# Kernel tuning notes

Hardware: AMD Instinct MI355X
Metric: run time of the kernel (lower is better)

Reference implementation:

```python
import jax, jax.numpy as jnp
import numpy as np

B, T, C, V = 4, 2048, 512, 32000


def setup_inputs() -> dict:
    key = jax.random.key(0)
    ks = jax.random.split(key, 8)
    return {
        "idx": jax.random.randint(ks[0], (B, T), 0, V, dtype=jnp.int64 if jax.config.jax_enable_x64 else jnp.int32),
        "targets": jax.random.randint(ks[1], (B, T), 0, V, dtype=jnp.int64 if jax.config.jax_enable_x64 else jnp.int32),
        "token_emb": jax.random.normal(ks[2], (V, C), jnp.float32) * 0.02,
        "pos_emb": jax.random.normal(ks[3], (T, C), jnp.float32) * 0.02,
        "Wk": jax.random.normal(ks[4], (C, C), jnp.float32) / np.sqrt(C),
        "Wq": jax.random.normal(ks[5], (C, C), jnp.float32) / np.sqrt(C),
        "Wv": jax.random.normal(ks[6], (C, C), jnp.float32) / np.sqrt(C),
        "Wo": jax.random.normal(ks[7], (C, V), jnp.float32) / np.sqrt(C),
        "bo": jnp.zeros((V,), jnp.float32),
    }


def reference(idx, targets, token_emb, pos_emb, Wk, Wq, Wv, Wo, bo):
    # embeddings: token lookup + positional add  -> [B, T, C]
    x = token_emb[idx] + pos_emb[None, :idx.shape[1]]
    # single self-attention head (scale uses input dim C, per source)
    q = x @ Wq  # [B, T, C]
    k = x @ Wk
    v = x @ Wv
    wei = jnp.einsum("btc,bsc->bts", q, k) * (C ** -0.5)  # [B, T, T]
    mask = jnp.tril(jnp.ones((idx.shape[1], idx.shape[1]), bool))
    wei = jnp.where(mask[None], wei, -jnp.inf)
    wei = jax.nn.softmax(wei, axis=-1)
    attn = jnp.einsum("bts,bsc->btc", wei, v)  # [B, T, C]
    logits = attn @ Wo + bo  # [B, T, V]
    # cross-entropy (mean over B*T), matching F.cross_entropy
    logp = jax.nn.log_softmax(logits, axis=-1)
    nll = -jnp.take_along_axis(logp, targets[..., None], axis=-1)[..., 0]
    loss = nll.mean()
    return logits, loss
```

## Files before the change

kernel.cpp:

```cpp
#include <hip/hip_runtime.h>
#include <cstdint>

typedef unsigned short u16;
typedef __attribute__((ext_vector_type(8))) short short8;
typedef __attribute__((ext_vector_type(4))) float f32x4;

constexpr int kB = 4, kT = 2048, kC = 512, kV = 32000;
constexpr int kBT = kB * kT;
constexpr float kScale = 0.044194173824159216f;

__device__ __forceinline__ u16 f2b(float f) {
  union { float f; unsigned u; } v; v.f = f;
  unsigned r = v.u + 0x7fffu + ((v.u >> 16) & 1u);
  return (u16)(r >> 16);
}

__device__ __forceinline__ void g2lds16(const u16* g, u16* l) {
  __builtin_amdgcn_global_load_lds(
      (const __attribute__((address_space(1))) void*)g,
      (__attribute__((address_space(3))) void*)l, 16, 0, 0);
}

__global__ __launch_bounds__(256) void transpose_cast(const float* __restrict__ in,
                                                      u16* __restrict__ out,
                                                      int R, int Ncol) {
  __shared__ u16 tile[32][33];
  int c0 = blockIdx.x * 32, r0 = blockIdx.y * 32;
  int tx = threadIdx.x, ty = threadIdx.y;
#pragma unroll
  for (int j = 0; j < 32; j += 8)
    tile[ty + j][tx] = f2b(in[(long)(r0 + ty + j) * Ncol + (c0 + tx)]);
  __syncthreads();
#pragma unroll
  for (int j = 0; j < 32; j += 8)
    out[(long)(c0 + ty + j) * R + (r0 + tx)] = tile[tx][ty + j];
}

__global__ __launch_bounds__(128) void embed_kernel(const int* __restrict__ idx,
                                                    const float* __restrict__ te,
                                                    const float* __restrict__ pe,
                                                    u16* __restrict__ xb) {
  int row = blockIdx.x;
  int t = row & (kT - 1);
  int tok = idx[row];
  int c = threadIdx.x * 4;
  float4 a = *(const float4*)(te + (long)tok * kC + c);
  float4 p = *(const float4*)(pe + (long)t * kC + c);
  ushort4 o;
  o.x = f2b(a.x + p.x); o.y = f2b(a.y + p.y);
  o.z = f2b(a.z + p.z); o.w = f2b(a.w + p.w);
  *(ushort4*)(xb + (long)row * kC + c) = o;
}

template <int OUT_MODE, bool CAUSAL>
__global__ __launch_bounds__(256) void gemm_bt(
    const u16* __restrict__ A, const u16* __restrict__ Bt, void* __restrict__ OutP,
    const float* __restrict__ bias,
    int M, int N, int K, int lda, int ldb, int ldo,
    long batchA, long batchB, long batchO, float alpha) {
  int bz = blockIdx.z;
  A += bz * batchA;
  Bt += bz * batchB;
  int m0 = blockIdx.y * 128, n0 = blockIdx.x * 128;
  if (CAUSAL && n0 > m0 + 127) return;

  __shared__ u16 As[2][128 * 32];
  __shared__ u16 Bs[2][128 * 32];
  int tid = threadIdx.x;
  int lane = tid & 63, w = tid >> 6;
  int wr = w >> 1, wc = w & 1;
  int lm = lane & 15, lk = lane >> 4;

  f32x4 acc[4][4] = {};

  const u16* aptr = A + (long)(m0 + (w << 4) + (lane >> 2)) * lda + ((lane & 3) << 3);
  const u16* bptr = Bt + (long)(n0 + (w << 4) + (lane >> 2)) * ldb + ((lane & 3) << 3);

#define STAGE(buf)                                                   \
  {                                                                  \
    g2lds16(aptr,                  &As[buf][(w << 4) * 32]);         \
    g2lds16(aptr + (long)64 * lda, &As[buf][(64 + (w << 4)) * 32]);  \
    g2lds16(bptr,                  &Bs[buf][(w << 4) * 32]);         \
    g2lds16(bptr + (long)64 * ldb, &Bs[buf][(64 + (w << 4)) * 32]);  \
  }

  int nk = K >> 5;
  STAGE(0);
  __syncthreads();

  for (int kt = 0; kt < nk; ++kt) {
    int cur = kt & 1;
    aptr += 32; bptr += 32;
    if (kt + 1 < nk) STAGE(cur ^ 1);
    short8 af[4], bf[4];
#pragma unroll
    for (int i = 0; i < 4; ++i) {
      af[i] = *(const short8*)&As[cur][(wr * 64 + i * 16 + lm) * 32 + lk * 8];
      bf[i] = *(const short8*)&Bs[cur][(wc * 64 + i * 16 + lm) * 32 + lk * 8];
    }
#pragma unroll
    for (int mi = 0; mi < 4; ++mi)
#pragma unroll
      for (int ni = 0; ni < 4; ++ni)
        acc[mi][ni] = __builtin_amdgcn_mfma_f32_16x16x32_bf16(af[mi], bf[ni], acc[mi][ni], 0, 0, 0);
    __syncthreads();
  }
#undef STAGE

#pragma unroll
  for (int mi = 0; mi < 4; ++mi) {
#pragma unroll
    for (int ni = 0; ni < 4; ++ni) {
      int row = m0 + wr * 64 + mi * 16 + lk * 4;
      int col = n0 + wc * 64 + ni * 16 + lm;
      if (OUT_MODE == 0) {
        float* Out = (float*)OutP + bz * batchO;
        float bv = bias ? bias[col] : 0.0f;
#pragma unroll
        for (int r = 0; r < 4; ++r)
          Out[(long)(row + r) * ldo + col] = acc[mi][ni][r] * alpha + bv;
      } else if (OUT_MODE == 1) {
        u16* Out = (u16*)OutP + bz * batchO;
#pragma unroll
        for (int r = 0; r < 4; ++r)
          Out[(long)(row + r) * ldo + col] = f2b(acc[mi][ni][r] * alpha);
      } else {
        u16* Out = (u16*)OutP + bz * batchO;
        ushort4 pk;
        pk.x = f2b(acc[mi][ni][0] * alpha);
        pk.y = f2b(acc[mi][ni][1] * alpha);
        pk.z = f2b(acc[mi][ni][2] * alpha);
        pk.w = f2b(acc[mi][ni][3] * alpha);
        *(ushort4*)&Out[(long)col * ldo + row] = pk;
      }
    }
  }
}

__global__ __launch_bounds__(512, 2) void gemm256_logits_ce(
    const u16* __restrict__ A, const u16* __restrict__ Bt,
    float* __restrict__ Out, const float* __restrict__ bias,
    float2* __restrict__ cepart) {
  constexpr int lda = kC, ldb = kC, ldo = kV;
  constexpr int nk = kC / 64;
  constexpr int NB = kV / 256;

  __shared__ u16 lds[65536];

  int wg = blockIdx.x;
  int swzb = (wg & 7) * (gridDim.x >> 3) + (wg >> 3);
  int bx = swzb % NB, by = swzb / NB;
  int m0 = by * 256, n0 = bx * 256;

  int tid = threadIdx.x;
  int lane = tid & 63, w = tid >> 6;
  int wm = w >> 2, wn = w & 3;
  int lm = lane & 15, lk = lane >> 4;
  int lk16 = lk * 16, sw = (lm & 7) << 4;
  int brow0 = (wn & 1) * 64;

  int srow = tid >> 3;
  int scol = ((tid & 7) ^ ((tid >> 3) & 7)) * 8;
  const u16* Arow = A + (long)(m0 + srow) * lda + scol;
  const u16* Brow = Bt + (long)(n0 + srow) * ldb + scol;

  f32x4 acc[8][4] = {};
  short8 aF[4][2], bF[4][2];

  auto stage = [&](int s) {
    if (s >= 4 * nk) return;
    int tile = s >> 2, hf = s & 3, buf = tile & 1;
    int kofs = tile * 64;
    if (hf >= 2) {
      u16* base = &lds[(buf * 2 + (hf - 2)) * 8192 + w * 512];
      const u16* g = Arow + (long)((hf - 2) * 128) * lda + kofs;
      g2lds16(g, base);
      g2lds16(g + (long)64 * lda, base + 4096);
    } else {
      u16* base = &lds[32768 + (buf * 2 + hf) * 8192 + w * 512];
      const u16* g = Brow + (long)(hf * 128) * ldb + kofs;
      g2lds16(g, base);
      g2lds16(g + (long)64 * ldb, base + 4096);
    }
  };

#pragma unroll
  for (int s = 0; s < 6; ++s) stage(s);
  asm volatile("s_waitcnt vmcnt(4)" ::: "memory");
  __builtin_amdgcn_sched_barrier(0);
  __builtin_amdgcn_s_barrier();

#pragma unroll 2
  for (int t = 0; t < nk; ++t) {
    int cur = t & 1;
    const char* Ab = (const char*)&lds[(cur * 2 + wm) * 8192];
    const char* Bb = (const char*)&lds[32768 + (cur * 2 + (wn >> 1)) * 8192];

#define RDA(i, ks) (*(const short8*)(Ab + (((qr)*4 + (i)) * 16 + lm) * 128 + (((ks)*64 + lk16) ^ sw)))
#define RDB(j, ks) (*(const short8*)(Bb + (brow0 + ((qc)*2 + (j)) * 16 + lm) * 128 + (((ks)*64 + lk16) ^ sw)))
#define MFMA_QUAD                                                              \
  _Pragma("unroll") for (int i = 0; i < 4; ++i)                                \
  _Pragma("unroll") for (int j = 0; j < 2; ++j)                                \
  _Pragma("unroll") for (int ks = 0; ks < 2; ++ks)                             \
      acc[qr * 4 + i][qc * 2 + j] = __builtin_amdgcn_mfma_f32_16x16x32_bf16(   \
          aF[i][ks], bF[qc * 2 + j][ks], acc[qr * 4 + i][qc * 2 + j], 0, 0, 0);

    {
      constexpr int qr = 0, qc = 0;
#pragma unroll
      for (int i = 0; i < 4; ++i) { aF[i][0] = RDA(i, 0); aF[i][1] = RDA(i, 1); }
#pragma unroll
      for (int j = 0; j < 2; ++j) { bF[j][0] = RDB(j, 0); bF[j][1] = RDB(j, 1); }
      stage(4 * (t + 1) + 2);
      stage(4 * (t + 1) + 3);
      __builtin_amdgcn_s_barrier();
      asm volatile("s_waitcnt lgkmcnt(0)" ::: "memory");
      __builtin_amdgcn_s_setprio(1);
      MFMA_QUAD
      __builtin_amdgcn_s_setprio(0);
      __builtin_amdgcn_s_barrier();
    }
    {
      constexpr int qr = 0, qc = 1;
#pragma unroll
      for (int j = 0; j < 2; ++j) { bF[2 + j][0] = RDB(j, 0); bF[2 + j][1] = RDB(j, 1); }
      __builtin_amdgcn_s_barrier();
      asm volatile("s_waitcnt lgkmcnt(0)" ::: "memory");
      __builtin_amdgcn_s_setprio(1);
      MFMA_QUAD
      __builtin_amdgcn_s_setprio(0);
      __builtin_amdgcn_s_barrier();
    }
    {
      constexpr int qr = 1, qc = 0;
#pragma unroll
      for (int i = 0; i < 4; ++i) { aF[i][0] = RDA(i, 0); aF[i][1] = RDA(i, 1); }
      __builtin_amdgcn_s_barrier();
      asm volatile("s_waitcnt lgkmcnt(0)" ::: "memory");
      __builtin_amdgcn_s_setprio(1);
      MFMA_QUAD
      __builtin_amdgcn_s_setprio(0);
      __builtin_amdgcn_s_barrier();
    }
    {
      constexpr int qr = 1, qc = 1;
      stage(4 * (t + 2) + 0);
      stage(4 * (t + 2) + 1);
      __builtin_amdgcn_s_barrier();
      asm volatile("s_waitcnt lgkmcnt(0)" ::: "memory");
      __builtin_amdgcn_s_setprio(1);
      MFMA_QUAD
      __builtin_amdgcn_s_setprio(0);
      if (t < nk - 2) {
        asm volatile("s_waitcnt vmcnt(4)" ::: "memory");
        __builtin_amdgcn_sched_barrier(0);
      } else if (t == nk - 2) {
        asm volatile("s_waitcnt vmcnt(0)" ::: "memory");
        __builtin_amdgcn_sched_barrier(0);
      }
      __builtin_amdgcn_s_barrier();
    }
#undef RDA
#undef RDB
#undef MFMA_QUAD
  }

  float2* lds_ce = (float2*)lds;
#pragma unroll
  for (int rf = 0; rf < 8; ++rf) {
    int grow = m0 + wm * 128 + rf * 16 + lk * 4;
    float rm[4], rs[4];
#pragma unroll
    for (int r = 0; r < 4; ++r) { rm[r] = -1e30f; rs[r] = 0.0f; }
#pragma unroll
    for (int cf = 0; cf < 4; ++cf) {
      int col = n0 + wn * 64 + cf * 16 + lm;
      float bv = bias[col];
#pragma unroll
      for (int r = 0; r < 4; ++r) {
        float v = acc[rf][cf][r] + bv;
        Out[(long)(grow + r) * ldo + col] = v;
        float M = fmaxf(rm[r], v);
        rs[r] = rs[r] * __expf(rm[r] - M) + __expf(v - M);
        rm[r] = M;
      }
    }
#pragma unroll
    for (int off = 1; off < 16; off <<= 1) {
#pragma unroll
      for (int r = 0; r < 4; ++r) {
        float om = __shfl_xor(rm[r], off, 64);
        float os = __shfl_xor(rs[r], off, 64);
        float M = fmaxf(rm[r], om);
        rs[r] = rs[r] * __expf(rm[r] - M) + os * __expf(om - M);
        rm[r] = M;
      }
    }
    if (lm == 0) {
#pragma unroll
      for (int r = 0; r < 4; ++r)
        lds_ce[w * 128 + rf * 16 + lk * 4 + r] = make_float2(rm[r], rs[r]);
    }
  }
  __syncthreads();
  if (tid < 256) {
    int row = tid, wmg = row >> 7, r128 = row & 127;
    float m = -1e30f, s = 0.0f;
#pragma unroll
    for (int j = 0; j < 4; ++j) {
      float2 v = lds_ce[(wmg * 4 + j) * 128 + r128];
      float M = fmaxf(m, v.x);
      s = s * __expf(m - M) + v.y * __expf(v.x - M);
      m = M;
    }
    cepart[(long)(m0 + row) * NB + bx] = make_float2(m, s);
  }
}

__global__ __launch_bounds__(256) void softmax_causal(const float* __restrict__ S,
                                                      u16* __restrict__ P) {
  int row = blockIdx.x;
  int t = row & (kT - 1);
  const float* srow = S + (long)row * kT;
  u16* prow = P + (long)row * kT;
  __shared__ float buf[kT];
  __shared__ float red[256];
  int tid = threadIdx.x;
  float mx = -1e30f;
  for (int s = tid; s < kT; s += 256) {
    float v = (s <= t) ? srow[s] : -1e30f;
    buf[s] = v;
    mx = fmaxf(mx, v);
  }
  red[tid] = mx; __syncthreads();
  for (int o = 128; o > 0; o >>= 1) {
    if (tid < o) red[tid] = fmaxf(red[tid], red[tid + o]);
    __syncthreads();
  }
  mx = red[0]; __syncthreads();
  float sm = 0.0f;
  for (int s = tid; s < kT; s += 256) {
    float e = (s <= t) ? __expf(buf[s] - mx) : 0.0f;
    buf[s] = e;
    sm += e;
  }
  red[tid] = sm; __syncthreads();
  for (int o = 128; o > 0; o >>= 1) {
    if (tid < o) red[tid] += red[tid + o];
    __syncthreads();
  }
  float inv = 1.0f / red[0];
  for (int s = tid; s < kT; s += 256) prow[s] = f2b(buf[s] * inv);
}

__global__ __launch_bounds__(256) void ce_reduce(const float* __restrict__ logits,
                                                 const float2* __restrict__ part,
                                                 const int* __restrict__ targets,
                                                 float* __restrict__ nll, int P) {
  int row = blockIdx.x * 4 + (threadIdx.x >> 6);
  int lane = threadIdx.x & 63;
  const float2* pr = part + (long)row * P;
  float m = -1e30f, s = 0.0f;
  for (int p = lane; p < P; p += 64) {
    float2 v = pr[p];
    float M = fmaxf(m, v.x);
    s = s * __expf(m - M) + v.y * __expf(v.x - M);
    m = M;
  }
#pragma unroll
  for (int off = 1; off < 64; off <<= 1) {
    float om = __shfl_xor(m, off, 64), os = __shfl_xor(s, off, 64);
    float M = fmaxf(m, om);
    s = s * __expf(m - M) + os * __expf(om - M);
    m = M;
  }
  if (lane == 0) {
    float lse = m + __logf(s);
    nll[row] = lse - logits[(long)row * kV + targets[row]];
  }
}

__global__ __launch_bounds__(256) void loss_reduce(const float* __restrict__ nll,
                                                   float* __restrict__ out) {
  __shared__ float red[256];
  int tid = threadIdx.x;
  float s = 0.0f;
  for (int i = tid; i < kBT; i += 256) s += nll[i];
  red[tid] = s; __syncthreads();
  for (int o = 128; o > 0; o >>= 1) {
    if (tid < o) red[tid] += red[tid + o];
    __syncthreads();
  }
  if (tid == 0) out[0] = red[0] / (float)kBT;
}

extern "C" void kernel_launch(void* const* d_in, const int* in_sizes, int n_in,
                              void* d_out, int out_size, void* d_ws, size_t ws_size,
                              hipStream_t stream) {
  const int* idx       = (const int*)d_in[0];
  const int* targets   = (const int*)d_in[1];
  const float* token_e = (const float*)d_in[2];
  const float* pos_e   = (const float*)d_in[3];
  const float* Wk      = (const float*)d_in[4];
  const float* Wq      = (const float*)d_in[5];
  const float* Wv      = (const float*)d_in[6];
  const float* Wo      = (const float*)d_in[7];
  const float* bo      = (const float*)d_in[8];
  float* out = (float*)d_out;

  char* ws = (char*)d_ws;
  size_t need = 0;
  auto alloc = [&](size_t bytes) { char* p = ws + need; need += (bytes + 255) & ~(size_t)255; return p; };
  u16* xb   = (u16*)alloc((size_t)kBT * kC * 2);
  u16* wqt  = (u16*)alloc((size_t)kC * kC * 2);
  u16* wkt  = (u16*)alloc((size_t)kC * kC * 2);
  u16* wvt  = (u16*)alloc((size_t)kC * kC * 2);
  u16* wot  = (u16*)alloc((size_t)kV * kC * 2);
  u16* qb   = (u16*)alloc((size_t)kBT * kC * 2);
  u16* kb   = (u16*)alloc((size_t)kBT * kC * 2);
  u16* vt   = (u16*)alloc((size_t)kC * kBT * 2);
  u16* attn = (u16*)alloc((size_t)kBT * kC * 2);
  float* nll = (float*)alloc((size_t)kBT * 4);
  if (ws_size < need) return;

  float2* cepart = (float2*)qb;

  float* Sbuf = out;
  u16* Pbuf   = (u16*)((char*)d_out + (100ull << 20));

  dim3 tb(32, 8);
  transpose_cast<<<dim3(kC / 32, kC / 32), tb, 0, stream>>>(Wq, wqt, kC, kC);
  transpose_cast<<<dim3(kC / 32, kC / 32), tb, 0, stream>>>(Wk, wkt, kC, kC);
  transpose_cast<<<dim3(kC / 32, kC / 32), tb, 0, stream>>>(Wv, wvt, kC, kC);
  transpose_cast<<<dim3(kV / 32, kC / 32), tb, 0, stream>>>(Wo, wot, kC, kV);

  embed_kernel<<<kBT, 128, 0, stream>>>(idx, token_e, pos_e, xb);

  gemm_bt<1, false><<<dim3(4, 64, 1), 256, 0, stream>>>(xb, wqt, qb, nullptr,
      kBT, kC, kC, kC, kC, kC, 0, 0, 0, 1.0f);
  gemm_bt<1, false><<<dim3(4, 64, 1), 256, 0, stream>>>(xb, wkt, kb, nullptr,
      kBT, kC, kC, kC, kC, kC, 0, 0, 0, 1.0f);
  gemm_bt<2, false><<<dim3(4, 64, 1), 256, 0, stream>>>(xb, wvt, vt, nullptr,
      kBT, kC, kC, kC, kC, kBT, 0, 0, 0, 1.0f);

  gemm_bt<0, true><<<dim3(16, 16, 4), 256, 0, stream>>>(qb, kb, Sbuf, nullptr,
      kT, kT, kC, kC, kC, kT, (long)kT * kC, (long)kT * kC, (long)kT * kT, kScale);

  softmax_causal<<<kBT, 256, 0, stream>>>(Sbuf, Pbuf);

  gemm_bt<1, false><<<dim3(4, 16, 4), 256, 0, stream>>>(Pbuf, vt, attn, nullptr,
      kT, kC, kT, kT, kBT, kC, (long)kT * kT, (long)kT, (long)kT * kC, 1.0f);

  gemm256_logits_ce<<<dim3((kV / 256) * (kBT / 256)), 512, 0, stream>>>(
      attn, wot, out, bo, cepart);

  ce_reduce<<<kBT / 4, 256, 0, stream>>>(out, cepart, targets, nll, kV / 256);
  loss_reduce<<<1, 256, 0, stream>>>(nll, out + (long)kBT * kV);
}
```

Measured before the change: 673.8 us.

## Skip masked causal work, merge Q/K projections, remap logits tiles, nontemporal stores

The P·V GEMM now caps its K loop at the causal limit for each 128-row tile, and the causal softmax only reads and writes up to the next 128-aligned column, so the fully masked upper triangle is skipped. Entries beyond that limit in the probability buffer are never written, which is safe only because the capped GEMM never reads them. The Q and K projections run as one batched launch, which assumes the wkt/wqt and kb/qb buffers sit contiguously. The logits+CE GEMM gets an explicit XCD-aware tile mapping that keeps row tiles of a chiplet together for L2 reuse. Its logits output uses nontemporal stores so the streamed output does not pollute the cache.

```diff
diff --git a/kernel.cpp b/kernel.cpp
--- a/kernel.cpp
+++ b/kernel.cpp
@@ -52,7 +52,7 @@
   *(ushort4*)(xb + (long)row * kC + c) = o;
 }
 
-template <int OUT_MODE, bool CAUSAL>
+template <int OUT_MODE, bool CAUSAL, bool KCAP>
 __global__ __launch_bounds__(256) void gemm_bt(
     const u16* __restrict__ A, const u16* __restrict__ Bt, void* __restrict__ OutP,
     const float* __restrict__ bias,
@@ -85,6 +85,7 @@
   }
 
   int nk = K >> 5;
+  if (KCAP) { int cap = (m0 >> 5) + 4; nk = (cap < nk) ? cap : nk; }
   STAGE(0);
   __syncthreads();
 
@@ -148,8 +149,11 @@
   __shared__ u16 lds[65536];
 
   int wg = blockIdx.x;
-  int swzb = (wg & 7) * (gridDim.x >> 3) + (wg >> 3);
-  int bx = swzb % NB, by = swzb / NB;
+  int xcd = wg & 7;
+  int i = wg >> 3;
+  int g = i >> 5, r = i & 31;
+  int bx = (g < 15) ? (g * 8 + (r >> 2)) : (120 + (r >> 2));
+  int by = xcd * 4 + (r & 3);
   int m0 = by * 256, n0 = bx * 256;
 
   int tid = threadIdx.x;
@@ -173,14 +177,14 @@
     int kofs = tile * 64;
     if (hf >= 2) {
       u16* base = &lds[(buf * 2 + (hf - 2)) * 8192 + w * 512];
-      const u16* g = Arow + (long)((hf - 2) * 128) * lda + kofs;
-      g2lds16(g, base);
-      g2lds16(g + (long)64 * lda, base + 4096);
+      const u16* gp = Arow + (long)((hf - 2) * 128) * lda + kofs;
+      g2lds16(gp, base);
+      g2lds16(gp + (long)64 * lda, base + 4096);
     } else {
       u16* base = &lds[32768 + (buf * 2 + hf) * 8192 + w * 512];
-      const u16* g = Brow + (long)(hf * 128) * ldb + kofs;
-      g2lds16(g, base);
-      g2lds16(g + (long)64 * ldb, base + 4096);
+      const u16* gp = Brow + (long)(hf * 128) * ldb + kofs;
+      g2lds16(gp, base);
+      g2lds16(gp + (long)64 * ldb, base + 4096);
     }
   };
 
@@ -279,7 +283,7 @@
 #pragma unroll
       for (int r = 0; r < 4; ++r) {
         float v = acc[rf][cf][r] + bv;
-        Out[(long)(grow + r) * ldo + col] = v;
+        __builtin_nontemporal_store(v, &Out[(long)(grow + r) * ldo + col]);
         float M = fmaxf(rm[r], v);
         rs[r] = rs[r] * __expf(rm[r] - M) + __expf(v - M);
         rm[r] = M;
@@ -321,13 +325,14 @@
                                                       u16* __restrict__ P) {
   int row = blockIdx.x;
   int t = row & (kT - 1);
+  int lim = ((t >> 7) + 1) << 7;
   const float* srow = S + (long)row * kT;
   u16* prow = P + (long)row * kT;
   __shared__ float buf[kT];
   __shared__ float red[256];
   int tid = threadIdx.x;
   float mx = -1e30f;
-  for (int s = tid; s < kT; s += 256) {
+  for (int s = tid; s < lim; s += 256) {
     float v = (s <= t) ? srow[s] : -1e30f;
     buf[s] = v;
     mx = fmaxf(mx, v);
@@ -339,7 +344,7 @@
   }
   mx = red[0]; __syncthreads();
   float sm = 0.0f;
-  for (int s = tid; s < kT; s += 256) {
+  for (int s = tid; s < lim; s += 256) {
     float e = (s <= t) ? __expf(buf[s] - mx) : 0.0f;
     buf[s] = e;
     sm += e;
@@ -350,7 +355,7 @@
     __syncthreads();
   }
   float inv = 1.0f / red[0];
-  for (int s = tid; s < kT; s += 256) prow[s] = f2b(buf[s] * inv);
+  for (int s = tid; s < lim; s += 256) prow[s] = f2b(buf[s] * inv);
 }
 
 __global__ __launch_bounds__(256) void ce_reduce(const float* __restrict__ logits,
@@ -436,19 +441,17 @@
 
   embed_kernel<<<kBT, 128, 0, stream>>>(idx, token_e, pos_e, xb);
 
-  gemm_bt<1, false><<<dim3(4, 64, 1), 256, 0, stream>>>(xb, wqt, qb, nullptr,
-      kBT, kC, kC, kC, kC, kC, 0, 0, 0, 1.0f);
-  gemm_bt<1, false><<<dim3(4, 64, 1), 256, 0, stream>>>(xb, wkt, kb, nullptr,
-      kBT, kC, kC, kC, kC, kC, 0, 0, 0, 1.0f);
-  gemm_bt<2, false><<<dim3(4, 64, 1), 256, 0, stream>>>(xb, wvt, vt, nullptr,
+  gemm_bt<1, false, false><<<dim3(4, 64, 2), 256, 0, stream>>>(xb, wqt, qb, nullptr,
+      kBT, kC, kC, kC, kC, kC, 0, (long)kC * kC, (long)kBT * kC, 1.0f);
+  gemm_bt<2, false, false><<<dim3(4, 64, 1), 256, 0, stream>>>(xb, wvt, vt, nullptr,
       kBT, kC, kC, kC, kC, kBT, 0, 0, 0, 1.0f);
 
-  gemm_bt<0, true><<<dim3(16, 16, 4), 256, 0, stream>>>(qb, kb, Sbuf, nullptr,
+  gemm_bt<0, true, false><<<dim3(16, 16, 4), 256, 0, stream>>>(qb, kb, Sbuf, nullptr,
       kT, kT, kC, kC, kC, kT, (long)kT * kC, (long)kT * kC, (long)kT * kT, kScale);
 
   softmax_causal<<<kBT, 256, 0, stream>>>(Sbuf, Pbuf);
 
-  gemm_bt<1, false><<<dim3(4, 16, 4), 256, 0, stream>>>(Pbuf, vt, attn, nullptr,
+  gemm_bt<1, false, true><<<dim3(4, 16, 4), 256, 0, stream>>>(Pbuf, vt, attn, nullptr,
       kT, kC, kT, kT, kBT, kC, (long)kT * kT, (long)kT, (long)kT * kC, 1.0f);
 
   gemm256_logits_ce<<<dim3((kV / 256) * (kBT / 256)), 512, 0, stream>>>(
```

Measured after the change: 611.6 us. 1.1x faster.
